# Kernel optimization log

Hardware: AMD Instinct MI355X
Metric: run time of the kernel (lower is better)

## Reference

```python
import jax, jax.numpy as jnp
import numpy as np

N = 20000   # num_nodes
R = 32      # num_relations
H = 64      # hidden_size
C = 8       # num_classes
E = 640000  # num_edges


def setup_inputs() -> dict:
    key = jax.random.key(0)
    k = jax.random.split(key, 8)
    edge_index = jax.random.randint(k[0], (2, E), 0, N, dtype=jnp.int64)
    edge_type = jnp.sort(jax.random.randint(k[1], (E,), 0, R, dtype=jnp.int64))
    # offsets per relation into the sorted edge list (R+1 entries)
    tensor_slice = jnp.searchsorted(edge_type, jnp.arange(R + 1)).astype(jnp.int64)
    # conv1: x=None => weight is a per-relation node-embedding table [R, N, H]
    W1 = jax.random.normal(k[2], (R, N, H), dtype=jnp.float32) * (1.0 / np.sqrt(N))
    root1 = jax.random.normal(k[3], (N, H), dtype=jnp.float32) * (1.0 / np.sqrt(N))
    bias1 = jnp.zeros((H,), dtype=jnp.float32)
    W2 = jax.random.normal(k[4], (R, H, C), dtype=jnp.float32) * (1.0 / np.sqrt(H))
    root2 = jax.random.normal(k[5], (H, C), dtype=jnp.float32) * (1.0 / np.sqrt(H))
    bias2 = jnp.zeros((C,), dtype=jnp.float32)
    return {"edge_index": edge_index, "edge_type": edge_type, "tensor_slice": tensor_slice,
            "W1": W1, "root1": root1, "bias1": bias1,
            "W2": W2, "root2": root2, "bias2": bias2}


def reference(edge_index, edge_type, tensor_slice, W1, root1, bias1, W2, root2, bias2):
    src, dst = edge_index[0], edge_index[1]
    # ---- conv1 (x = None): message for edge e is row W1[edge_type[e], src[e]]
    msg1 = W1[edge_type, src]                                   # [E, H] gather
    h = jax.ops.segment_sum(msg1, dst, num_segments=N)          # scatter-add (aggr='add')
    h = h + root1 + bias1                                       # root term = root1[node] since x=None
    h = jax.nn.relu(h)
    # ---- conv2: transform all nodes under every relation once, then gather per edge
    h_rel = jnp.einsum('nh,rhc->rnc', h, W2)                    # [R, N, C]
    msg2 = h_rel[edge_type, src]                                # [E, C] gather
    out = jax.ops.segment_sum(msg2, dst, num_segments=N)        # [N, C]
    out = out + h @ root2 + bias2
    return jax.nn.log_softmax(out, axis=1)
```

## Files before the change

kernel.cpp:

```cpp
#include <hip/hip_runtime.h>
#include <math.h>

#define NN 20000
#define RR 32
#define HH 64
#define CC 8
#define EE 640000
#define CAP 128
#define RT 8

__global__ __launch_bounds__(256) void k_zero(int* __restrict__ cnt) {
    int i = blockIdx.x * 256 + threadIdx.x;
    if (i < NN) cnt[i] = 0;
}

__global__ __launch_bounds__(256) void k_scatter(const int* __restrict__ ei,
                                                 const int* __restrict__ et,
                                                 int* __restrict__ cnt,
                                                 unsigned* __restrict__ pk2) {
    int e = (blockIdx.x * 256 + threadIdx.x) * 4;
    if (e >= EE) return;
    int4 sv = *(const int4*)(ei + e);
    int4 dv = *(const int4*)(ei + EE + e);
    int4 rv = *(const int4*)(et + e);
    int s0 = atomicAdd(&cnt[dv.x], 1);
    int s1 = atomicAdd(&cnt[dv.y], 1);
    int s2 = atomicAdd(&cnt[dv.z], 1);
    int s3 = atomicAdd(&cnt[dv.w], 1);
    pk2[((size_t)dv.x << 7) + s0] = (unsigned)sv.x | ((unsigned)rv.x << 15);
    pk2[((size_t)dv.y << 7) + s1] = (unsigned)sv.y | ((unsigned)rv.y << 15);
    pk2[((size_t)dv.z << 7) + s2] = (unsigned)sv.z | ((unsigned)rv.z << 15);
    pk2[((size_t)dv.w << 7) + s3] = (unsigned)sv.w | ((unsigned)rv.w << 15);
}

__global__ __launch_bounds__(256) void k_gather1(const unsigned* __restrict__ pk2,
                                                 const int* __restrict__ cnt,
                                                 const float* __restrict__ W1,
                                                 const float* __restrict__ root1,
                                                 const float* __restrict__ bias1,
                                                 const float* __restrict__ root2,
                                                 float* __restrict__ h,
                                                 float* __restrict__ outr) {
    int wid = (blockIdx.x * 256 + threadIdx.x) >> 6;
    int lane = threadIdx.x & 63;
    if (wid >= NN) return;
    const int eg = lane >> 4;
    const int q  = lane & 15;
    float4 acc4 = make_float4(0.f, 0.f, 0.f, 0.f);
    int beg = wid << 7;
    int end = beg + cnt[wid];
    int i = beg;
    for (; i + 16 <= end; i += 16) {
        unsigned p0 = pk2[i + eg], p1 = pk2[i + 4 + eg];
        unsigned p2 = pk2[i + 8 + eg], p3 = pk2[i + 12 + eg];
        float4 w0 = *((const float4*)(W1 + ((size_t)(p0 >> 15) * NN + (p0 & 0x7fffu)) * HH) + q);
        float4 w1 = *((const float4*)(W1 + ((size_t)(p1 >> 15) * NN + (p1 & 0x7fffu)) * HH) + q);
        float4 w2 = *((const float4*)(W1 + ((size_t)(p2 >> 15) * NN + (p2 & 0x7fffu)) * HH) + q);
        float4 w3 = *((const float4*)(W1 + ((size_t)(p3 >> 15) * NN + (p3 & 0x7fffu)) * HH) + q);
        acc4.x += (w0.x + w1.x) + (w2.x + w3.x);
        acc4.y += (w0.y + w1.y) + (w2.y + w3.y);
        acc4.z += (w0.z + w1.z) + (w2.z + w3.z);
        acc4.w += (w0.w + w1.w) + (w2.w + w3.w);
    }
    for (; i + 4 <= end; i += 4) {
        unsigned p = pk2[i + eg];
        float4 w = *((const float4*)(W1 + ((size_t)(p >> 15) * NN + (p & 0x7fffu)) * HH) + q);
        acc4.x += w.x; acc4.y += w.y; acc4.z += w.z; acc4.w += w.w;
    }
    acc4.x += __shfl_xor(acc4.x, 16); acc4.y += __shfl_xor(acc4.y, 16);
    acc4.z += __shfl_xor(acc4.z, 16); acc4.w += __shfl_xor(acc4.w, 16);
    acc4.x += __shfl_xor(acc4.x, 32); acc4.y += __shfl_xor(acc4.y, 32);
    acc4.z += __shfl_xor(acc4.z, 32); acc4.w += __shfl_xor(acc4.w, 32);
    int sl = lane >> 2;
    float cx = __shfl(acc4.x, sl), cy = __shfl(acc4.y, sl);
    float cz = __shfl(acc4.z, sl), cw = __shfl(acc4.w, sl);
    int comp = lane & 3;
    float acc = cx;
    if (comp == 1) acc = cy;
    if (comp == 2) acc = cz;
    if (comp == 3) acc = cw;
    for (; i < end; ++i) {
        unsigned p = pk2[i];
        acc += W1[((size_t)(p >> 15) * NN + (p & 0x7fffu)) * HH + lane];
    }
    acc += root1[(size_t)wid * HH + lane] + bias1[lane];
    float hv = fmaxf(acc, 0.0f);
    h[(size_t)wid * HH + lane] = hv;
    float4 ra = *(const float4*)(root2 + lane * CC);
    float4 rb = *(const float4*)(root2 + lane * CC + 4);
    float a0 = hv * ra.x, a1 = hv * ra.y, a2 = hv * ra.z, a3 = hv * ra.w;
    float a4 = hv * rb.x, a5 = hv * rb.y, a6 = hv * rb.z, a7 = hv * rb.w;
    #pragma unroll
    for (int m = 1; m < 8; m <<= 1) {
        a0 += __shfl_xor(a0, m); a1 += __shfl_xor(a1, m);
        a2 += __shfl_xor(a2, m); a3 += __shfl_xor(a3, m);
        a4 += __shfl_xor(a4, m); a5 += __shfl_xor(a5, m);
        a6 += __shfl_xor(a6, m); a7 += __shfl_xor(a7, m);
    }
    int c = lane & 7;
    float v = a0;
    if (c == 1) v = a1;  if (c == 2) v = a2;  if (c == 3) v = a3;
    if (c == 4) v = a4;  if (c == 5) v = a5;  if (c == 6) v = a6;
    if (c == 7) v = a7;
    v += __shfl_xor(v, 8);
    v += __shfl_xor(v, 16);
    v += __shfl_xor(v, 32);
    if (lane < 8) outr[(size_t)wid * CC + lane] = v;
}

__global__ __launch_bounds__(256) void k_hrel(const float* __restrict__ h,
                                              const float* __restrict__ W2,
                                              float* __restrict__ hrel) {
    __shared__ float w2s[RT * HH * CC];
    int r0 = blockIdx.y * RT;
    int tid = threadIdx.x;
    #pragma unroll
    for (int u = 0; u < RT * HH * CC / 256; u++)
        w2s[u * 256 + tid] = W2[(size_t)r0 * HH * CC + u * 256 + tid];
    __syncthreads();
    int n = blockIdx.x * 256 + tid;
    if (n >= NN) return;
    const float* hp = h + (size_t)n * HH;
    float4 hreg[HH / 4];
    #pragma unroll
    for (int k4 = 0; k4 < HH / 4; k4++) hreg[k4] = ((const float4*)hp)[k4];
    for (int rr = 0; rr < RT; rr++) {
        const float* w = w2s + rr * HH * CC;
        float acc[CC] = {0, 0, 0, 0, 0, 0, 0, 0};
        #pragma unroll
        for (int k4 = 0; k4 < HH / 4; k4++) {
            float4 hv = hreg[k4];
            int k = k4 * 4;
            #pragma unroll
            for (int c = 0; c < CC; c++) {
                acc[c] += hv.x * w[(k + 0) * CC + c] + hv.y * w[(k + 1) * CC + c]
                        + hv.z * w[(k + 2) * CC + c] + hv.w * w[(k + 3) * CC + c];
            }
        }
        float* op = hrel + ((size_t)(r0 + rr) * NN + n) * CC;
        *(float4*)(op)     = make_float4(acc[0], acc[1], acc[2], acc[3]);
        *(float4*)(op + 4) = make_float4(acc[4], acc[5], acc[6], acc[7]);
    }
}

__global__ __launch_bounds__(256) void k_gather2(const unsigned* __restrict__ pk2,
                                                 const int* __restrict__ cnt,
                                                 const float* __restrict__ hrel,
                                                 const float* __restrict__ outr,
                                                 const float* __restrict__ bias2,
                                                 float* __restrict__ out) {
    int wid = (blockIdx.x * 256 + threadIdx.x) >> 6;
    int lane = threadIdx.x & 63;
    if (wid >= NN) return;
    int eg = lane >> 1, half = lane & 1;
    float4 acc = make_float4(0.f, 0.f, 0.f, 0.f);
    int beg = wid << 7;
    int end = beg + cnt[wid];
    for (int i = beg + eg; i < end; i += 32) {
        unsigned p = pk2[i];
        float4 v = *((const float4*)(hrel + ((size_t)(p >> 15) * NN + (p & 0x7fffu)) * CC) + half);
        acc.x += v.x; acc.y += v.y; acc.z += v.z; acc.w += v.w;
    }
    #pragma unroll
    for (int m = 2; m < 64; m <<= 1) {
        acc.x += __shfl_xor(acc.x, m);
        acc.y += __shfl_xor(acc.y, m);
        acc.z += __shfl_xor(acc.z, m);
        acc.w += __shfl_xor(acc.w, m);
    }
    float4 o = *((const float4*)(outr + (size_t)wid * CC) + half);
    float4 b = *((const float4*)bias2 + half);
    float4 x;
    x.x = acc.x + o.x + b.x;
    x.y = acc.y + o.y + b.y;
    x.z = acc.z + o.z + b.z;
    x.w = acc.w + o.w + b.w;
    float m4 = fmaxf(fmaxf(x.x, x.y), fmaxf(x.z, x.w));
    float mm = fmaxf(m4, __shfl_xor(m4, 1));
    float e4 = expf(x.x - mm) + expf(x.y - mm) + expf(x.z - mm) + expf(x.w - mm);
    float ss = e4 + __shfl_xor(e4, 1);
    float l = mm + logf(ss);
    if (lane < 2) {
        float4 r = make_float4(x.x - l, x.y - l, x.z - l, x.w - l);
        *((float4*)(out + (size_t)wid * CC) + half) = r;
    }
}

extern "C" void kernel_launch(void* const* d_in, const int* in_sizes, int n_in,
                              void* d_out, int out_size, void* d_ws, size_t ws_size,
                              hipStream_t stream) {
    const int*   ei    = (const int*)d_in[0];
    const int*   et    = (const int*)d_in[1];
    const float* W1    = (const float*)d_in[3];
    const float* root1 = (const float*)d_in[4];
    const float* bias1 = (const float*)d_in[5];
    const float* W2    = (const float*)d_in[6];
    const float* root2 = (const float*)d_in[7];
    const float* bias2 = (const float*)d_in[8];
    float* out = (float*)d_out;

    char* base = (char*)d_ws;
    int*      cnt  = (int*)(base);
    unsigned* pk2  = (unsigned*)(base + 80128);
    float*    h    = (float*)(base + 10320128);
    float*    outr = (float*)(base + 15440128);
    float*    hrel = (float*)(base + 16080128);

    k_zero   <<<(NN + 255) / 256, 256, 0, stream>>>(cnt);
    k_scatter<<<(EE / 4 + 255) / 256, 256, 0, stream>>>(ei, et, cnt, pk2);
    k_gather1<<<(NN * 64 + 255) / 256, 256, 0, stream>>>(pk2, cnt, W1, root1, bias1, root2, h, outr);
    k_hrel   <<<dim3((NN + 255) / 256, RR / RT), 256, 0, stream>>>(h, W2, hrel);
    k_gather2<<<(NN * 64 + 255) / 256, 256, 0, stream>>>(pk2, cnt, hrel, outr, bias2, out);
}
```

Baseline: 124.9 us.

## Fuse per-relation h transform into gather1 and store hrel node-major

Removes the separate k_hrel kernel and the h buffer. Each wavefront now computes all 32x8 relation outputs for its node right after the ReLU, broadcasting h with shuffles and reading W2 straight from global/cache. hrel is relaid out as [N, R, C], so gather2 reads it at a per-node 1KB row offset by relation. This saves one launch and the h round trip through memory. In exchange gather1 does 64 dependent shuffle+FMA steps per lane and loads W2 without shared memory.

```diff
diff --git a/kernel.cpp b/kernel.cpp
--- a/kernel.cpp
+++ b/kernel.cpp
@@ -7,7 +7,6 @@
 #define CC 8
 #define EE 640000
 #define CAP 128
-#define RT 8
 
 __global__ __launch_bounds__(256) void k_zero(int* __restrict__ cnt) {
     int i = blockIdx.x * 256 + threadIdx.x;
@@ -39,7 +38,8 @@
                                                  const float* __restrict__ root1,
                                                  const float* __restrict__ bias1,
                                                  const float* __restrict__ root2,
-                                                 float* __restrict__ h,
+                                                 const float* __restrict__ W2,
+                                                 float* __restrict__ hrel,
                                                  float* __restrict__ outr) {
     int wid = (blockIdx.x * 256 + threadIdx.x) >> 6;
     int lane = threadIdx.x & 63;
@@ -85,7 +85,6 @@
     }
     acc += root1[(size_t)wid * HH + lane] + bias1[lane];
     float hv = fmaxf(acc, 0.0f);
-    h[(size_t)wid * HH + lane] = hv;
     float4 ra = *(const float4*)(root2 + lane * CC);
     float4 rb = *(const float4*)(root2 + lane * CC + 4);
     float a0 = hv * ra.x, a1 = hv * ra.y, a2 = hv * ra.z, a3 = hv * ra.w;
@@ -106,41 +105,16 @@
     v += __shfl_xor(v, 16);
     v += __shfl_xor(v, 32);
     if (lane < 8) outr[(size_t)wid * CC + lane] = v;
-}
-
-__global__ __launch_bounds__(256) void k_hrel(const float* __restrict__ h,
-                                              const float* __restrict__ W2,
-                                              float* __restrict__ hrel) {
-    __shared__ float w2s[RT * HH * CC];
-    int r0 = blockIdx.y * RT;
-    int tid = threadIdx.x;
+    int r = lane >> 1, hf = lane & 1;
+    const float* w2p = W2 + (size_t)r * HH * CC + hf * 4;
+    float4 a8 = make_float4(0.f, 0.f, 0.f, 0.f);
     #pragma unroll
-    for (int u = 0; u < RT * HH * CC / 256; u++)
-        w2s[u * 256 + tid] = W2[(size_t)r0 * HH * CC + u * 256 + tid];
-    __syncthreads();
-    int n = blockIdx.x * 256 + tid;
-    if (n >= NN) return;
-    const float* hp = h + (size_t)n * HH;
-    float4 hreg[HH / 4];
-    #pragma unroll
-    for (int k4 = 0; k4 < HH / 4; k4++) hreg[k4] = ((const float4*)hp)[k4];
-    for (int rr = 0; rr < RT; rr++) {
-        const float* w = w2s + rr * HH * CC;
-        float acc[CC] = {0, 0, 0, 0, 0, 0, 0, 0};
-        #pragma unroll
-        for (int k4 = 0; k4 < HH / 4; k4++) {
-            float4 hv = hreg[k4];
-            int k = k4 * 4;
-            #pragma unroll
-            for (int c = 0; c < CC; c++) {
-                acc[c] += hv.x * w[(k + 0) * CC + c] + hv.y * w[(k + 1) * CC + c]
-                        + hv.z * w[(k + 2) * CC + c] + hv.w * w[(k + 3) * CC + c];
-            }
-        }
-        float* op = hrel + ((size_t)(r0 + rr) * NN + n) * CC;
-        *(float4*)(op)     = make_float4(acc[0], acc[1], acc[2], acc[3]);
-        *(float4*)(op + 4) = make_float4(acc[4], acc[5], acc[6], acc[7]);
+    for (int k = 0; k < HH; k++) {
+        float bk = __shfl(hv, k);
+        float4 wv = *(const float4*)(w2p + k * CC);
+        a8.x += bk * wv.x; a8.y += bk * wv.y; a8.z += bk * wv.z; a8.w += bk * wv.w;
     }
+    *((float4*)(hrel + (size_t)wid * (RR * CC)) + lane) = a8;
 }
 
 __global__ __launch_bounds__(256) void k_gather2(const unsigned* __restrict__ pk2,
@@ -158,7 +132,7 @@
     int end = beg + cnt[wid];
     for (int i = beg + eg; i < end; i += 32) {
         unsigned p = pk2[i];
-        float4 v = *((const float4*)(hrel + ((size_t)(p >> 15) * NN + (p & 0x7fffu)) * CC) + half);
+        float4 v = *((const float4*)(hrel + (size_t)(p & 0x7fffu) * (RR * CC)) + ((p >> 15) << 1) + half);
         acc.x += v.x; acc.y += v.y; acc.z += v.z; acc.w += v.w;
     }
     #pragma unroll
@@ -202,13 +176,11 @@
     char* base = (char*)d_ws;
     int*      cnt  = (int*)(base);
     unsigned* pk2  = (unsigned*)(base + 80128);
-    float*    h    = (float*)(base + 10320128);
-    float*    outr = (float*)(base + 15440128);
-    float*    hrel = (float*)(base + 16080128);
+    float*    outr = (float*)(base + 10320128);
+    float*    hrel = (float*)(base + 10960128);
 
     k_zero   <<<(NN + 255) / 256, 256, 0, stream>>>(cnt);
     k_scatter<<<(EE / 4 + 255) / 256, 256, 0, stream>>>(ei, et, cnt, pk2);
-    k_gather1<<<(NN * 64 + 255) / 256, 256, 0, stream>>>(pk2, cnt, W1, root1, bias1, root2, h, outr);
-    k_hrel   <<<dim3((NN + 255) / 256, RR / RT), 256, 0, stream>>>(h, W2, hrel);
+    k_gather1<<<(NN * 64 + 255) / 256, 256, 0, stream>>>(pk2, cnt, W1, root1, bias1, root2, W2, hrel, outr);
     k_gather2<<<(NN * 64 + 255) / 256, 256, 0, stream>>>(pk2, cnt, hrel, outr, bias2, out);
 }
```

Result: slower. 151.3 us (+21.2%).
